# Kernel tuning notes

Measured on AMD Instinct MI355X. Metric: run time of the kernel, lower is better.

The kernel has to match this reference:

```python
import jax, jax.numpy as jnp
import numpy as np

B, N, M, D, H, DFF = 1, 2048, 2048, 1024, 16, 4096
MASK_VAL = -50000.0
EPS = 1e-5


def _xavier(k, shape):
    lim = np.sqrt(6.0 / (shape[0] + shape[1])).astype(np.float32)
    return jax.random.uniform(k, shape, jnp.float32, -lim, lim)


def setup_inputs() -> dict:
    key = jax.random.key(0)
    ks = jax.random.split(key, 8)
    return {
        "x": jax.random.normal(ks[0], (B, N, D), jnp.float32),
        "context": jax.random.normal(ks[1], (B, M, D), jnp.float32),
        "Wq": _xavier(ks[2], (D, D)), "bq": jnp.zeros((D,), jnp.float32),
        "Wkv": _xavier(ks[3], (D, 2 * D)), "bkv": jnp.zeros((2 * D,), jnp.float32),
        "Wo": _xavier(ks[4], (D, D)), "bo": jnp.zeros((D,), jnp.float32),
        "ln1_g": jnp.ones((D,), jnp.float32), "ln1_b": jnp.zeros((D,), jnp.float32),
        "W1": _xavier(ks[5], (D, DFF)), "bf1": jnp.zeros((DFF,), jnp.float32),
        "W2": _xavier(ks[6], (DFF, D)), "bf2": jnp.zeros((D,), jnp.float32),
        "ln2_g": jnp.ones((D,), jnp.float32), "ln2_b": jnp.zeros((D,), jnp.float32),
    }


def _layernorm(x, g, b):
    mu = x.mean(-1, keepdims=True)
    var = ((x - mu) ** 2).mean(-1, keepdims=True)
    return (x - mu) * jax.lax.rsqrt(var + EPS) * g + b


def reference(x, context, Wq, bq, Wkv, bkv, Wo, bo, ln1_g, ln1_b, W1, bf1, W2, bf2, ln2_g, ln2_b):
    b, n, d = x.shape
    m = context.shape[1]
    h = H
    dh = d // h
    scale = dh ** -0.5
    # q from x only; k,v from [x; context]
    q = (x @ Wq + bq).reshape(b, n, h, dh).transpose(0, 2, 1, 3)          # b h n dh
    kv_in = jnp.concatenate([x, context], axis=1)                          # b (n+m) d
    k, v = jnp.split(kv_in @ Wkv + bkv, 2, axis=-1)
    k = k.reshape(b, n + m, h, dh).transpose(0, 2, 1, 3)                   # b h (n+m) dh
    v = v.reshape(b, n + m, h, dh).transpose(0, 2, 1, 3)
    dots = jnp.einsum('bhid,bhjd->bhij', q * scale, k)                     # b h n (n+m)
    # causal mask applies only to the self-attention (first n) key columns
    rows = jnp.arange(n)[:, None]
    cols = jnp.arange(n + m)[None, :]
    causal = (cols < n) & (cols > rows)
    dots = jnp.where(causal, MASK_VAL, dots)
    attn = jax.nn.softmax(dots, axis=-1)                                   # dropout = identity (eval)
    out = jnp.einsum('bhij,bhjd->bhid', attn, v)
    out = out.transpose(0, 2, 1, 3).reshape(b, n, d) @ Wo + bo
    # PostNorm(Residual(attn))
    x1 = _layernorm(x + out, ln1_g, ln1_b)
    # PostNorm(Residual(FFN)) with exact-erf GELU
    ff = jax.nn.gelu(x1 @ W1 + bf1, approximate=False) @ W2 + bf2
    return _layernorm(x1 + ff, ln2_g, ln2_b)
```

## Files before the change

### kernel.cpp

```cpp
#include <hip/hip_runtime.h>


using bf16x8 = __attribute__((ext_vector_type(8))) short;
using f32x4  = __attribute__((ext_vector_type(4))) float;

__device__ __forceinline__ ushort f2bf(float f) {
    unsigned u = __float_as_uint(f);
    unsigned r = (u + 0x7fffu + ((u >> 16) & 1u)) >> 16;
    return (ushort)r;
}

__device__ __forceinline__ float bf2f(ushort u) {
    return __uint_as_float((uint)u << 16);
}

__device__ __forceinline__ void gload16(const void* g, void* l) {
    __builtin_amdgcn_global_load_lds(
        (const __attribute__((address_space(1))) void*)g,
        (__attribute__((address_space(3))) void*)l, 16, 0, 0);
}

__device__ __forceinline__ float gelu_erf(float v) {
    return 0.5f * v * (1.0f + erff(v * 0.70710678118654752f));
}

__device__ __forceinline__ uint cvtpk(float a, float b) {
    uint r;
    asm("v_cvt_pk_bf16_f32 %0, %1, %2" : "=v"(r) : "v"(a), "v"(b));
    return r;
}

__global__ __launch_bounds__(256) void prep_all(
    const float* __restrict__ x, const float* __restrict__ ctx,
    ushort* __restrict__ XCb,
    const float* __restrict__ Wq, const float* __restrict__ Wkv,
    const float* __restrict__ Wo, const float* __restrict__ W1,
    const float* __restrict__ W2,
    ushort* __restrict__ WqT, ushort* __restrict__ WkvT,
    ushort* __restrict__ WoT, ushort* __restrict__ W1T,
    ushort* __restrict__ W2T) {
    __shared__ float tile[32][33];
    int b = blockIdx.x;
    if (b < 4096) {
        const float* in = (b < 2048) ? x : ctx;
        ushort* out = XCb + ((b < 2048) ? 0 : (size_t)2048 * 1024);
        const int i = ((b & 2047) * 256 + threadIdx.x) * 4;
        float4 v = *(const float4*)(in + i);
        ushort4 o;
        o.x = f2bf(v.x); o.y = f2bf(v.y); o.z = f2bf(v.z); o.w = f2bf(v.w);
        *(ushort4*)(out + i) = o;
        return;
    }
    b -= 4096;
    const float* in; ushort* out; int R, C, loc;
    if (b < 1024)      { in = Wq;  out = WqT;  R = 1024; C = 1024; loc = b; }
    else if (b < 3072) { in = Wkv; out = WkvT; R = 1024; C = 2048; loc = b - 1024; }
    else if (b < 4096) { in = Wo;  out = WoT;  R = 1024; C = 1024; loc = b - 3072; }
    else if (b < 8192) { in = W1;  out = W1T;  R = 1024; C = 4096; loc = b - 4096; }
    else               { in = W2;  out = W2T;  R = 4096; C = 1024; loc = b - 8192; }
    const int nbx = C >> 5;
    const int c0 = (loc % nbx) * 32, r0 = (loc / nbx) * 32;
    const int tx = threadIdx.x & 31, ty = threadIdx.x >> 5;
#pragma unroll
    for (int i = 0; i < 4; ++i)
        tile[ty + 8 * i][tx] = in[(size_t)(r0 + ty + 8 * i) * C + c0 + tx];
    __syncthreads();
#pragma unroll
    for (int i = 0; i < 4; ++i)
        out[(size_t)(c0 + ty + 8 * i) * R + r0 + tx] = f2bf(tile[tx][ty + 8 * i]);
}

template <int BM, int BN, int ACT, int OUTF32, int RES, int SCALED, int SPLITK, int VT>
__global__ __launch_bounds__(256) void gemm_bt(
    const ushort* __restrict__ A, int lda, const ushort* __restrict__ Bt, int ldb,
    const float* __restrict__ bias, const float* __restrict__ resid,
    void* __restrict__ Cout, ushort* __restrict__ Vout,
    int M, int N, int K, float scale) {
    constexpr int MR = BM / 32, NR = BN / 32;
    __shared__ __align__(16) ushort Asm[BM * 64];
    __shared__ __align__(16) ushort Bsm[BN * 64];
    const int tid = threadIdx.x;
    const int w = tid >> 6, lane = tid & 63, g = lane >> 4, i15 = lane & 15;
    const int wm = w >> 1, wn = w & 1;
    const int m0 = blockIdx.y * BM, n0 = blockIdx.x * BN;
    if (SPLITK) {
        A += (size_t)blockIdx.z * K;
        Bt += (size_t)blockIdx.z * K;
    }

    f32x4 acc[MR][NR] = {};

    for (int kt = 0; kt < K; kt += 64) {
#pragma unroll
        for (int q = 0; q < BM / 32; ++q) {
            int off = (w * (BM / 32) + q) * 1024 + lane * 16;
            int r = off >> 7, cb = off & 127;
            int scb = cb ^ ((r & 7) << 4);
            const void* src = (const char*)A + ((size_t)(m0 + r) * lda + kt) * 2 + scb;
            gload16(src, (char*)Asm + (w * (BM / 32) + q) * 1024);
        }
#pragma unroll
        for (int q = 0; q < BN / 32; ++q) {
            int off = (w * (BN / 32) + q) * 1024 + lane * 16;
            int r = off >> 7, cb = off & 127;
            int scb = cb ^ ((r & 7) << 4);
            const void* src = (const char*)Bt + ((size_t)(n0 + r) * ldb + kt) * 2 + scb;
            gload16(src, (char*)Bsm + (w * (BN / 32) + q) * 1024);
        }
        __syncthreads();

#pragma unroll
        for (int kc = 0; kc < 2; ++kc) {
            bf16x8 af[MR], bfr[NR];
#pragma unroll
            for (int mi = 0; mi < MR; ++mi) {
                int r = wm * (BM / 2) + mi * 16 + i15;
                af[mi] = *(const bf16x8*)((const char*)Asm + r * 128 +
                                          ((kc * 64 + g * 16) ^ ((r & 7) << 4)));
            }
#pragma unroll
            for (int ni = 0; ni < NR; ++ni) {
                int r = wn * (BN / 2) + ni * 16 + i15;
                bfr[ni] = *(const bf16x8*)((const char*)Bsm + r * 128 +
                                           ((kc * 64 + g * 16) ^ ((r & 7) << 4)));
            }
#pragma unroll
            for (int mi = 0; mi < MR; ++mi)
#pragma unroll
                for (int ni = 0; ni < NR; ++ni)
                    acc[mi][ni] = __builtin_amdgcn_mfma_f32_16x16x32_bf16(
                        af[mi], bfr[ni], acc[mi][ni], 0, 0, 0);
        }
        __syncthreads();
    }

    float* Cf = (float*)Cout;
    ushort* Cb = (ushort*)Cout;
    if (SPLITK) {
        Cf += (size_t)blockIdx.z * M * N;
        Cb += (size_t)blockIdx.z * M * N;
    }

#pragma unroll
    for (int ni = 0; ni < NR; ++ni) {
        int col = n0 + wn * (BN / 2) + ni * 16 + i15;
        float bb = bias ? bias[col] : 0.f;
#pragma unroll
        for (int mi = 0; mi < MR; ++mi) {
            if (VT && col >= 1024) {
                int row = m0 + wm * (BM / 2) + mi * 16 + 4 * g;
                ushort4 ov;
                ov.x = f2bf(acc[mi][ni][0] + bb);
                ov.y = f2bf(acc[mi][ni][1] + bb);
                ov.z = f2bf(acc[mi][ni][2] + bb);
                ov.w = f2bf(acc[mi][ni][3] + bb);
                *(ushort4*)(Vout + (size_t)(col - 1024) * 4096 + row) = ov;
            } else {
#pragma unroll
                for (int r2 = 0; r2 < 4; ++r2) {
                    int row = m0 + wm * (BM / 2) + mi * 16 + 4 * g + r2;
                    float v = acc[mi][ni][r2] + bb;
                    if (ACT) v = gelu_erf(v);
                    if (SCALED) v *= scale;
                    size_t off = VT ? ((size_t)row * 1024 + col)
                                    : ((size_t)row * N + col);
                    if (OUTF32) {
                        float rv = RES ? resid[off] : 0.f;
                        Cf[off] = v + rv;
                    } else {
                        Cb[off] = f2bf(v);
                    }
                }
            }
        }
    }
}

template <int NS>
__global__ __launch_bounds__(512) void flash_attn(
    const ushort* __restrict__ Q,
    const ushort* __restrict__ Kb,
    const ushort* __restrict__ Vt,
    ushort* __restrict__ O,
    ushort* __restrict__ Opart,
    float* __restrict__ Ml) {
    constexpr int D = 1024;
    __shared__ __align__(16) ushort Ksm[2][64 * 64];
    __shared__ __align__(16) ushort Vsm[2][64 * 64];
    __shared__ __align__(16) ushort Psm[8][16 * 64];

    const int tid = threadIdx.x;
    const int w = tid >> 6, lane = tid & 63, g = lane >> 4, i15 = lane & 15;
    const int bid = blockIdx.x;
    const int h = bid & 15;
    const int qB = 15 - ((bid >> 4) & 15);
    const int s = (NS > 1) ? (bid >> 8) : 0;
    const int qb = qB * 128 + w * 16;
    const int qrow = qb + i15;
    const int diagW = qb >> 6;
    const int diagB = 2 * qB + 1;
    const int nt = diagB + 33;
    const int lo = (s * nt) / NS;
    const int hi = ((s + 1) * nt) / NS;

    bf16x8 qf[2];
    qf[0] = *(const bf16x8*)(Q + (size_t)qrow * D + h * 64 + g * 8);
    qf[1] = *(const bf16x8*)(Q + (size_t)qrow * D + h * 64 + 32 + g * 8);

    const short oneb = (short)0x3F80;
    const bf16x8 ones = {oneb, oneb, oneb, oneb, oneb, oneb, oneb, oneb};

    f32x4 o[4] = {};
    f32x4 ls = {};
    float m_run = -INFINITY;

    const int sr  = tid >> 3;
    const int scb = (tid & 7) * 16;
    const int ssw = scb ^ ((sr & 7) << 4);
    const char* kb0 = (const char*)Kb + ((size_t)sr * 1024 + h * 64) * 2 + scb;
    const char* vb0 = (const char*)Vt + ((size_t)(h * 64 + sr) * 4096) * 2 + scb;

    uint4 kreg, vreg;
    auto jt_of = [&](int t) { return (t <= diagB) ? t : (32 + (t - diagB - 1)); };
    auto stage = [&](int t) {
        const int jt = jt_of(t);
        kreg = *(const uint4*)(kb0 + (size_t)jt * 64 * 2048);
        vreg = *(const uint4*)(vb0 + (size_t)jt * 128);
    };
    auto wlds = [&](int buf) {
        *(uint4*)((char*)Ksm[buf] + sr * 128 + ssw) = kreg;
        *(uint4*)((char*)Vsm[buf] + sr * 128 + ssw) = vreg;
    };

    const int pbase = i15 * 128;
    const int psw = (i15 & 7) << 4;

    auto body = [&](int buf, int t) {
        const int jt = jt_of(t);
        f32x4 st[4];
        __builtin_amdgcn_s_setprio(1);
#pragma unroll
        for (int jg = 0; jg < 4; ++jg) {
            int jr = jg * 16 + i15;
            bf16x8 ka0 = *(const bf16x8*)((const char*)Ksm[buf] + jr * 128 +
                                          ((g * 16) ^ ((jr & 7) << 4)));
            bf16x8 ka1 = *(const bf16x8*)((const char*)Ksm[buf] + jr * 128 +
                                          ((64 + g * 16) ^ ((jr & 7) << 4)));
            f32x4 z = {};
            z = __builtin_amdgcn_mfma_f32_16x16x32_bf16(ka0, qf[0], z, 0, 0, 0);
            z = __builtin_amdgcn_mfma_f32_16x16x32_bf16(ka1, qf[1], z, 0, 0, 0);
            st[jg] = z;
        }
        __builtin_amdgcn_s_setprio(0);
        if (jt >= diagW && jt <= diagB) {
#pragma unroll
            for (int jg = 0; jg < 4; ++jg)
#pragma unroll
                for (int r = 0; r < 4; ++r) {
                    int j = jt * 64 + jg * 16 + 4 * g + r;
                    if (j > qrow) st[jg][r] = -50000.f;
                }
        }

        float a0 = fmaxf(fmaxf(st[0][0], st[0][1]), st[0][2]);
        float a1 = fmaxf(fmaxf(st[0][3], st[1][0]), st[1][1]);
        float a2 = fmaxf(fmaxf(st[1][2], st[1][3]), st[2][0]);
        float a3 = fmaxf(fmaxf(st[2][1], st[2][2]), st[2][3]);
        float a4 = fmaxf(fmaxf(st[3][0], st[3][1]), st[3][2]);
        float b0 = fmaxf(fmaxf(a0, a1), a2);
        float b1 = fmaxf(fmaxf(a3, a4), st[3][3]);
        float mt = fmaxf(b0, b1);
        mt = fmaxf(mt, __shfl_xor(mt, 16));
        mt = fmaxf(mt, __shfl_xor(mt, 32));

        const bool skip = __all(mt - m_run <= 8.f);
        float mnew, fscale;
        if (skip) { mnew = m_run; fscale = 1.f; }
        else      { mnew = fmaxf(m_run, mt); fscale = exp2f(m_run - mnew); }

        float pf[4][4];
#pragma unroll
        for (int jg = 0; jg < 4; ++jg)
#pragma unroll
            for (int r = 0; r < 4; ++r) pf[jg][r] = exp2f(st[jg][r] - mnew);
        m_run = mnew;

        if (!skip) {
#pragma unroll
            for (int r = 0; r < 4; ++r) {
                float fr = __shfl(fscale, 20 * g + r);
#pragma unroll
                for (int dg = 0; dg < 4; ++dg) o[dg][r] *= fr;
                ls[r] *= fr;
            }
        }

#pragma unroll
        for (int jg = 0; jg < 4; ++jg) {
            uint2 pk;
            pk.x = cvtpk(pf[jg][0], pf[jg][1]);
            pk.y = cvtpk(pf[jg][2], pf[jg][3]);
            *(uint2*)((char*)Psm[w] + pbase + ((jg * 32 + g * 8) ^ psw)) = pk;
        }

        __builtin_amdgcn_s_setprio(1);
#pragma unroll
        for (int jc = 0; jc < 2; ++jc) {
            bf16x8 pa = *(const bf16x8*)((const char*)Psm[w] + pbase +
                                         ((jc * 64 + g * 16) ^ psw));
            ls = __builtin_amdgcn_mfma_f32_16x16x32_bf16(pa, ones, ls, 0, 0, 0);
#pragma unroll
            for (int dg = 0; dg < 4; ++dg) {
                int dr = dg * 16 + i15;
                bf16x8 vb = *(const bf16x8*)((const char*)Vsm[buf] + dr * 128 +
                                             ((jc * 64 + g * 16) ^ ((dr & 7) << 4)));
                o[dg] = __builtin_amdgcn_mfma_f32_16x16x32_bf16(pa, vb, o[dg], 0, 0, 0);
            }
        }
        __builtin_amdgcn_s_setprio(0);
    };

    stage(lo);
    wlds(0);
    __syncthreads();

    int t = lo;
    for (; t + 1 < hi; t += 2) {
        stage(t + 1);
        body(0, t);
        wlds(1);
        __syncthreads();
        if (t + 2 < hi) stage(t + 2);
        body(1, t + 1);
        if (t + 2 < hi) { wlds(0); __syncthreads(); }
    }
    if (t < hi) body(0, t);

    if (NS > 1) {
#pragma unroll
        for (int r = 0; r < 4; ++r) {
            if (i15 == 4 * g + r) {
                float* mp = Ml + ((size_t)(s * 2048 + qrow) * 16 + h) * 2;
                mp[0] = m_run; mp[1] = ls[r];
            }
        }
#pragma unroll
        for (int r = 0; r < 4; ++r)
#pragma unroll
            for (int dg = 0; dg < 4; ++dg) {
                int row = qb + 4 * g + r;
                int col = h * 64 + dg * 16 + i15;
                Opart[(size_t)(s * 2048 + row) * 1024 + col] = f2bf(o[dg][r]);
            }
    } else {
#pragma unroll
        for (int r = 0; r < 4; ++r) {
            float inv = 1.f / ls[r];
#pragma unroll
            for (int dg = 0; dg < 4; ++dg) {
                int row = qb + 4 * g + r;
                int col = h * 64 + dg * 16 + i15;
                O[(size_t)row * D + col] = f2bf(o[dg][r] * inv);
            }
        }
    }
}

template <int NS>
__global__ __launch_bounds__(256) void attn_combine(
    const ushort* __restrict__ Opart, const float* __restrict__ Ml,
    ushort* __restrict__ O) {
    const int row = blockIdx.x, tid = threadIdx.x;
    const int c = tid * 4, h = c >> 6;
    float ms[NS], lsv[NS];
#pragma unroll
    for (int s = 0; s < NS; ++s) {
        const float* mp = Ml + ((size_t)(s * 2048 + row) * 16 + h) * 2;
        ms[s] = mp[0]; lsv[s] = mp[1];
    }
    float m = ms[0];
#pragma unroll
    for (int s = 1; s < NS; ++s) m = fmaxf(m, ms[s]);
    float denom = 0.f, wgt[NS];
#pragma unroll
    for (int s = 0; s < NS; ++s) { wgt[s] = exp2f(ms[s] - m); denom += lsv[s] * wgt[s]; }
    const float inv = 1.f / denom;
    float ax = 0, ay = 0, az = 0, aw = 0;
#pragma unroll
    for (int s = 0; s < NS; ++s) {
        ushort4 a = *(const ushort4*)(Opart + (size_t)(s * 2048 + row) * 1024 + c);
        ax += bf2f(a.x) * wgt[s]; ay += bf2f(a.y) * wgt[s];
        az += bf2f(a.z) * wgt[s]; aw += bf2f(a.w) * wgt[s];
    }
    ushort4 ob;
    ob.x = f2bf(ax * inv); ob.y = f2bf(ay * inv);
    ob.z = f2bf(az * inv); ob.w = f2bf(aw * inv);
    *(ushort4*)(O + (size_t)row * 1024 + c) = ob;
}

__global__ __launch_bounds__(256) void layernorm_k(
    const float* __restrict__ in, const float* __restrict__ gam,
    const float* __restrict__ bet, float* __restrict__ outf,
    ushort* __restrict__ outb) {
    const int row = blockIdx.x, tid = threadIdx.x;
    const float4 v = *(const float4*)(in + (size_t)row * 1024 + tid * 4);
    float s = v.x + v.y + v.z + v.w;
    float sq = v.x * v.x + v.y * v.y + v.z * v.z + v.w * v.w;
#pragma unroll
    for (int d = 1; d < 64; d <<= 1) {
        s += __shfl_xor(s, d);
        sq += __shfl_xor(sq, d);
    }
    __shared__ float red[8];
    const int w = tid >> 6;
    if ((tid & 63) == 0) { red[w] = s; red[4 + w] = sq; }
    __syncthreads();
    s = red[0] + red[1] + red[2] + red[3];
    sq = red[4] + red[5] + red[6] + red[7];
    const float mu = s * (1.f / 1024.f);
    const float rs = rsqrtf(sq * (1.f / 1024.f) - mu * mu + 1e-5f);
    const float4 gg = *(const float4*)(gam + tid * 4);
    const float4 bb = *(const float4*)(bet + tid * 4);
    float4 o;
    o.x = (v.x - mu) * rs * gg.x + bb.x;
    o.y = (v.y - mu) * rs * gg.y + bb.y;
    o.z = (v.z - mu) * rs * gg.z + bb.z;
    o.w = (v.w - mu) * rs * gg.w + bb.w;
    *(float4*)(outf + (size_t)row * 1024 + tid * 4) = o;
    if (outb) {
        ushort4 ob;
        ob.x = f2bf(o.x); ob.y = f2bf(o.y); ob.z = f2bf(o.z); ob.w = f2bf(o.w);
        *(ushort4*)(outb + (size_t)row * 1024 + tid * 4) = ob;
    }
}

template <int NP, int PBF16, int OUTB>
__global__ __launch_bounds__(256) void layernorm_comb(
    const void* __restrict__ P,
    const float* __restrict__ bias, const float* __restrict__ resid,
    const float* __restrict__ gam, const float* __restrict__ bet,
    float* __restrict__ outf, ushort* __restrict__ outb) {
    const int row = blockIdx.x, tid = threadIdx.x;
    const float4 rr = *(const float4*)(resid + (size_t)row * 1024 + tid * 4);
    const float4 bs = *(const float4*)(bias + tid * 4);
    float4 v;
    v.x = rr.x + bs.x; v.y = rr.y + bs.y; v.z = rr.z + bs.z; v.w = rr.w + bs.w;
#pragma unroll
    for (int p = 0; p < NP; ++p) {
        if (PBF16) {
            ushort4 a = *(const ushort4*)((const ushort*)P +
                          (size_t)(p * 2048 + row) * 1024 + tid * 4);
            v.x += bf2f(a.x); v.y += bf2f(a.y); v.z += bf2f(a.z); v.w += bf2f(a.w);
        } else {
            float4 a = *(const float4*)((const float*)P +
                          (size_t)(p * 2048 + row) * 1024 + tid * 4);
            v.x += a.x; v.y += a.y; v.z += a.z; v.w += a.w;
        }
    }
    float s = v.x + v.y + v.z + v.w;
    float sq = v.x * v.x + v.y * v.y + v.z * v.z + v.w * v.w;
#pragma unroll
    for (int d = 1; d < 64; d <<= 1) {
        s += __shfl_xor(s, d);
        sq += __shfl_xor(sq, d);
    }
    __shared__ float red[8];
    const int w = tid >> 6;
    if ((tid & 63) == 0) { red[w] = s; red[4 + w] = sq; }
    __syncthreads();
    s = red[0] + red[1] + red[2] + red[3];
    sq = red[4] + red[5] + red[6] + red[7];
    const float mu = s * (1.f / 1024.f);
    const float rs = rsqrtf(sq * (1.f / 1024.f) - mu * mu + 1e-5f);
    const float4 gg = *(const float4*)(gam + tid * 4);
    const float4 bb = *(const float4*)(bet + tid * 4);
    float4 o;
    o.x = (v.x - mu) * rs * gg.x + bb.x;
    o.y = (v.y - mu) * rs * gg.y + bb.y;
    o.z = (v.z - mu) * rs * gg.z + bb.z;
    o.w = (v.w - mu) * rs * gg.w + bb.w;
    *(float4*)(outf + (size_t)row * 1024 + tid * 4) = o;
    if (OUTB) {
        ushort4 ob;
        ob.x = f2bf(o.x); ob.y = f2bf(o.y); ob.z = f2bf(o.z); ob.w = f2bf(o.w);
        *(ushort4*)(outb + (size_t)row * 1024 + tid * 4) = ob;
    }
}

extern "C" void kernel_launch(void* const* d_in, const int* in_sizes, int n_in,
                              void* d_out, int out_size, void* d_ws, size_t ws_size,
                              hipStream_t stream) {
    const float* x    = (const float*)d_in[0];
    const float* ctx  = (const float*)d_in[1];
    const float* Wq   = (const float*)d_in[2];
    const float* bq   = (const float*)d_in[3];
    const float* Wkv  = (const float*)d_in[4];
    const float* bkv  = (const float*)d_in[5];
    const float* Wo   = (const float*)d_in[6];
    const float* bo   = (const float*)d_in[7];
    const float* g1   = (const float*)d_in[8];
    const float* b1   = (const float*)d_in[9];
    const float* W1   = (const float*)d_in[10];
    const float* bf1  = (const float*)d_in[11];
    const float* W2   = (const float*)d_in[12];
    const float* bf2  = (const float*)d_in[13];
    const float* g2   = (const float*)d_in[14];
    const float* b2   = (const float*)d_in[15];

    char* ws = (char*)d_ws;
    const size_t MB = 1u << 20;
    ushort* XCb  = (ushort*)(ws + 0);
    ushort* WoT  = (ushort*)(ws + 8 * MB);
    ushort* W1T  = (ushort*)(ws + 10 * MB);
    ushort* W2T  = (ushort*)(ws + 18 * MB);
    ushort* WqT  = (ushort*)(ws + 26 * MB);
    ushort* WkvT = (ushort*)(ws + 28 * MB);
    ushort* Qs   = (ushort*)(ws + 32 * MB);
    ushort* attn = (ushort*)(ws + 36 * MB);
    ushort* Kb   = (ushort*)(ws + 40 * MB);
    ushort* Vt   = (ushort*)(ws + 48 * MB);
    ushort* x1b  = (ushort*)(ws + 26 * MB);
    float*  x1f  = (float*)(ws + 32 * MB);
    ushort* ffb  = (ushort*)(ws + 40 * MB);
    float*  y1   = (float*)(ws + 56 * MB);
    ushort* Opart = (ushort*)(ws + 64 * MB);
    float*  Pwo   = (float*)(ws + 64 * MB);
    ushort* Pk4b  = (ushort*)(ws + 64 * MB);
    float*  Pk2   = (float*)(ws + 0);
    float*  Ml    = (float*)(ws + 80 * MB);

    prep_all<<<16384, 256, 0, stream>>>(x, ctx, XCb, Wq, Wkv, Wo, W1, W2,
                                        WqT, WkvT, WoT, W1T, W2T);
    gemm_bt<64, 128, 0, 0, 0, 1, 0, 0><<<dim3(8, 32), 256, 0, stream>>>(
        XCb, 1024, WqT, 1024, bq, nullptr, Qs, nullptr,
        2048, 1024, 1024, 0.18033688011112042f);
    gemm_bt<128, 128, 0, 0, 0, 0, 0, 1><<<dim3(16, 32), 256, 0, stream>>>(
        XCb, 1024, WkvT, 1024, bkv, nullptr, Kb, Vt,
        4096, 2048, 1024, 1.f);

    const bool big = ws_size >= 82 * MB;
    if (big) {
        flash_attn<4><<<1024, 512, 0, stream>>>(Qs, Kb, Vt, nullptr, Opart, Ml);
        attn_combine<4><<<2048, 256, 0, stream>>>(Opart, Ml, attn);
        gemm_bt<64, 128, 0, 1, 0, 0, 1, 0><<<dim3(8, 32, 2), 256, 0, stream>>>(
            attn, 1024, WoT, 1024, nullptr, nullptr, Pwo, nullptr,
            2048, 1024, 512, 1.f);
        layernorm_comb<2, 0, 1><<<2048, 256, 0, stream>>>(
            Pwo, bo, x, g1, b1, x1f, x1b);
        gemm_bt<128, 128, 1, 0, 0, 0, 0, 0><<<dim3(32, 16), 256, 0, stream>>>(
            x1b, 1024, W1T, 1024, bf1, nullptr, ffb, nullptr,
            2048, 4096, 1024, 1.f);
        gemm_bt<128, 128, 0, 0, 0, 0, 1, 0><<<dim3(8, 16, 4), 256, 0, stream>>>(
            ffb, 4096, W2T, 4096, nullptr, nullptr, Pk4b, nullptr,
            2048, 1024, 1024, 1.f);
        layernorm_comb<4, 1, 0><<<2048, 256, 0, stream>>>(
            Pk4b, bf2, x1f, g2, b2, (float*)d_out, nullptr);
    } else {
        flash_attn<1><<<256, 512, 0, stream>>>(Qs, Kb, Vt, attn, nullptr, nullptr);
        gemm_bt<64, 128, 0, 1, 1, 0, 0, 0><<<dim3(8, 32), 256, 0, stream>>>(
            attn, 1024, WoT, 1024, bo, x, y1, nullptr, 2048, 1024, 1024, 1.f);
        layernorm_k<<<2048, 256, 0, stream>>>(y1, g1, b1, x1f, x1b);
        gemm_bt<128, 128, 1, 0, 0, 0, 0, 0><<<dim3(32, 16), 256, 0, stream>>>(
            x1b, 1024, W1T, 1024, bf1, nullptr, ffb, nullptr,
            2048, 4096, 1024, 1.f);
        gemm_bt<128, 128, 0, 1, 0, 0, 1, 0><<<dim3(8, 16, 2), 256, 0, stream>>>(
            ffb, 4096, W2T, 4096, nullptr, nullptr, Pk2, nullptr,
            2048, 1024, 2048, 1.f);
        layernorm_comb<2, 0, 0><<<2048, 256, 0, stream>>>(
            Pk2, bf2, x1f, g2, b2, (float*)d_out, nullptr);
    }
}
```

Measured before the change: 204.4 us.

## Fuse Q and KV projections into one GEMM launch; vectorize weight transpose

Replaces the separate Q projection GEMM and KV projection GEMM with a single gemm_qkv kernel. It uses a flat 640-block grid: 128 blocks cover the Q region over the first 2048 rows and 512 blocks cover the K/V region over all 4096 rows. Each block picks its output (scaled Q, K, or transposed V) from its column range. This removes one launch and lets both projections fill the GPU together. The weight-transpose prep now uses float4 loads and packed bf16 stores via v_cvt_pk_bf16_f32, cutting memory instructions. It assumes WqT and WkvT are contiguous in the workspace so one Bt pointer covers the concatenated 3072-column weight.

Result: no change. 207.0 us (+1.3%).

```diff
diff --git a/kernel.cpp b/kernel.cpp
--- a/kernel.cpp
+++ b/kernel.cpp
@@ -41,10 +41,11 @@
     ushort* __restrict__ W2T) {
     __shared__ float tile[32][33];
     int b = blockIdx.x;
+    const int t = threadIdx.x;
     if (b < 4096) {
         const float* in = (b < 2048) ? x : ctx;
         ushort* out = XCb + ((b < 2048) ? 0 : (size_t)2048 * 1024);
-        const int i = ((b & 2047) * 256 + threadIdx.x) * 4;
+        const int i = ((b & 2047) * 256 + t) * 4;
         float4 v = *(const float4*)(in + i);
         ushort4 o;
         o.x = f2bf(v.x); o.y = f2bf(v.y); o.z = f2bf(v.z); o.w = f2bf(v.w);
@@ -60,22 +61,27 @@
     else               { in = W2;  out = W2T;  R = 4096; C = 1024; loc = b - 8192; }
     const int nbx = C >> 5;
     const int c0 = (loc % nbx) * 32, r0 = (loc / nbx) * 32;
-    const int tx = threadIdx.x & 31, ty = threadIdx.x >> 5;
-#pragma unroll
-    for (int i = 0; i < 4; ++i)
-        tile[ty + 8 * i][tx] = in[(size_t)(r0 + ty + 8 * i) * C + c0 + tx];
+    {
+        const int r = t >> 3, c4 = (t & 7) * 4;
+        float4 v = *(const float4*)(in + (size_t)(r0 + r) * C + c0 + c4);
+        tile[r][c4] = v.x; tile[r][c4 + 1] = v.y;
+        tile[r][c4 + 2] = v.z; tile[r][c4 + 3] = v.w;
+    }
     __syncthreads();
-#pragma unroll
-    for (int i = 0; i < 4; ++i)
-        out[(size_t)(c0 + ty + 8 * i) * R + r0 + tx] = f2bf(tile[tx][ty + 8 * i]);
-}
-
-template <int BM, int BN, int ACT, int OUTF32, int RES, int SCALED, int SPLITK, int VT>
+    {
+        const int c = t >> 3, r4 = (t & 7) * 4;
+        uint2 pk;
+        pk.x = cvtpk(tile[r4][c], tile[r4 + 1][c]);
+        pk.y = cvtpk(tile[r4 + 2][c], tile[r4 + 3][c]);
+        *(uint2*)(out + (size_t)(c0 + c) * R + r0 + r4) = pk;
+    }
+}
+
+template <int BM, int BN, int ACT, int OUTF32, int RES, int SCALED, int SPLITK>
 __global__ __launch_bounds__(256) void gemm_bt(
     const ushort* __restrict__ A, int lda, const ushort* __restrict__ Bt, int ldb,
     const float* __restrict__ bias, const float* __restrict__ resid,
-    void* __restrict__ Cout, ushort* __restrict__ Vout,
-    int M, int N, int K, float scale) {
+    void* __restrict__ Cout, int M, int N, int K, float scale) {
     constexpr int MR = BM / 32, NR = BN / 32;
     __shared__ __align__(16) ushort Asm[BM * 64];
     __shared__ __align__(16) ushort Bsm[BN * 64];
@@ -147,28 +153,112 @@
         float bb = bias ? bias[col] : 0.f;
 #pragma unroll
         for (int mi = 0; mi < MR; ++mi) {
-            if (VT && col >= 1024) {
-                int row = m0 + wm * (BM / 2) + mi * 16 + 4 * g;
+#pragma unroll
+            for (int r2 = 0; r2 < 4; ++r2) {
+                int row = m0 + wm * (BM / 2) + mi * 16 + 4 * g + r2;
+                float v = acc[mi][ni][r2] + bb;
+                if (ACT) v = gelu_erf(v);
+                if (SCALED) v *= scale;
+                size_t off = (size_t)row * N + col;
+                if (OUTF32) {
+                    float rv = RES ? resid[off] : 0.f;
+                    Cf[off] = v + rv;
+                } else {
+                    Cb[off] = f2bf(v);
+                }
+            }
+        }
+    }
+}
+
+__global__ __launch_bounds__(256) void gemm_qkv(
+    const ushort* __restrict__ A,
+    const ushort* __restrict__ Bt,
+    const float* __restrict__ bq, const float* __restrict__ bkv,
+    ushort* __restrict__ Qs, ushort* __restrict__ Kb, ushort* __restrict__ Vt,
+    float qscale) {
+    constexpr int MR = 4, NR = 4;
+    __shared__ __align__(16) ushort Asm[128 * 64];
+    __shared__ __align__(16) ushort Bsm[128 * 64];
+    const int tid = threadIdx.x;
+    const int w = tid >> 6, lane = tid & 63, g = lane >> 4, i15 = lane & 15;
+    const int wm = w >> 1, wn = w & 1;
+    const int bid = blockIdx.x;
+    int bx, by;
+    if (bid < 128) { bx = bid & 7; by = bid >> 3; }
+    else { int b2 = bid - 128; bx = 8 + (b2 & 15); by = b2 >> 4; }
+    const int m0 = by * 128, n0 = bx * 128;
+    const int reg = (n0 < 1024) ? 0 : (n0 < 2048 ? 1 : 2);
+
+    f32x4 acc[MR][NR] = {};
+
+    for (int kt = 0; kt < 1024; kt += 64) {
+#pragma unroll
+        for (int q = 0; q < 4; ++q) {
+            int off = (w * 4 + q) * 1024 + lane * 16;
+            int r = off >> 7, cb = off & 127;
+            int scb = cb ^ ((r & 7) << 4);
+            const void* src = (const char*)A + ((size_t)(m0 + r) * 1024 + kt) * 2 + scb;
+            gload16(src, (char*)Asm + (w * 4 + q) * 1024);
+        }
+#pragma unroll
+        for (int q = 0; q < 4; ++q) {
+            int off = (w * 4 + q) * 1024 + lane * 16;
+            int r = off >> 7, cb = off & 127;
+            int scb = cb ^ ((r & 7) << 4);
+            const void* src = (const char*)Bt + ((size_t)(n0 + r) * 1024 + kt) * 2 + scb;
+            gload16(src, (char*)Bsm + (w * 4 + q) * 1024);
+        }
+        __syncthreads();
+
+#pragma unroll
+        for (int kc = 0; kc < 2; ++kc) {
+            bf16x8 af[MR], bfr[NR];
+#pragma unroll
+            for (int mi = 0; mi < MR; ++mi) {
+                int r = wm * 64 + mi * 16 + i15;
+                af[mi] = *(const bf16x8*)((const char*)Asm + r * 128 +
+                                          ((kc * 64 + g * 16) ^ ((r & 7) << 4)));
+            }
+#pragma unroll
+            for (int ni = 0; ni < NR; ++ni) {
+                int r = wn * 64 + ni * 16 + i15;
+                bfr[ni] = *(const bf16x8*)((const char*)Bsm + r * 128 +
+                                           ((kc * 64 + g * 16) ^ ((r & 7) << 4)));
+            }
+#pragma unroll
+            for (int mi = 0; mi < MR; ++mi)
+#pragma unroll
+                for (int ni = 0; ni < NR; ++ni)
+                    acc[mi][ni] = __builtin_amdgcn_mfma_f32_16x16x32_bf16(
+                        af[mi], bfr[ni], acc[mi][ni], 0, 0, 0);
+        }
+        __syncthreads();
+    }
+
+#pragma unroll
+    for (int ni = 0; ni < NR; ++ni) {
+        int col = n0 + wn * 64 + ni * 16 + i15;
+        float bb = (reg == 0) ? bq[col] : bkv[col - 1024];
+#pragma unroll
+        for (int mi = 0; mi < MR; ++mi) {
+            if (reg == 2) {
+                int row = m0 + wm * 64 + mi * 16 + 4 * g;
                 ushort4 ov;
                 ov.x = f2bf(acc[mi][ni][0] + bb);
                 ov.y = f2bf(acc[mi][ni][1] + bb);
                 ov.z = f2bf(acc[mi][ni][2] + bb);
                 ov.w = f2bf(acc[mi][ni][3] + bb);
-                *(ushort4*)(Vout + (size_t)(col - 1024) * 4096 + row) = ov;
+                *(ushort4*)(Vt + (size_t)(col - 2048) * 4096 + row) = ov;
             } else {
 #pragma unroll
                 for (int r2 = 0; r2 < 4; ++r2) {
-                    int row = m0 + wm * (BM / 2) + mi * 16 + 4 * g + r2;
+                    int row = m0 + wm * 64 + mi * 16 + 4 * g + r2;
                     float v = acc[mi][ni][r2] + bb;
-                    if (ACT) v = gelu_erf(v);
-                    if (SCALED) v *= scale;
-                    size_t off = VT ? ((size_t)row * 1024 + col)
-                                    : ((size_t)row * N + col);
-                    if (OUTF32) {
-                        float rv = RES ? resid[off] : 0.f;
-                        Cf[off] = v + rv;
+                    if (reg == 0) {
+                        Qs[(size_t)row * 1024 + col] = f2bf(v * qscale);
                     } else {
-                        Cb[off] = f2bf(v);
+                        Kb[(size_t)row * 1024 + (col - 1024)] = f2bf(v);
                     }
                 }
             }
@@ -531,41 +621,35 @@
 
     prep_all<<<16384, 256, 0, stream>>>(x, ctx, XCb, Wq, Wkv, Wo, W1, W2,
                                         WqT, WkvT, WoT, W1T, W2T);
-    gemm_bt<64, 128, 0, 0, 0, 1, 0, 0><<<dim3(8, 32), 256, 0, stream>>>(
-        XCb, 1024, WqT, 1024, bq, nullptr, Qs, nullptr,
-        2048, 1024, 1024, 0.18033688011112042f);
-    gemm_bt<128, 128, 0, 0, 0, 0, 0, 1><<<dim3(16, 32), 256, 0, stream>>>(
-        XCb, 1024, WkvT, 1024, bkv, nullptr, Kb, Vt,
-        4096, 2048, 1024, 1.f);
+    gemm_qkv<<<640, 256, 0, stream>>>(XCb, WqT, bq, bkv, Qs, Kb, Vt,
+                                      0.18033688011112042f);
 
     const bool big = ws_size >= 82 * MB;
     if (big) {
         flash_attn<4><<<1024, 512, 0, stream>>>(Qs, Kb, Vt, nullptr, Opart, Ml);
         attn_combine<4><<<2048, 256, 0, stream>>>(Opart, Ml, attn);
-        gemm_bt<64, 128, 0, 1, 0, 0, 1, 0><<<dim3(8, 32, 2), 256, 0, stream>>>(
-            attn, 1024, WoT, 1024, nullptr, nullptr, Pwo, nullptr,
+        gemm_bt<64, 128, 0, 1, 0, 0, 1><<<dim3(8, 32, 2), 256, 0, stream>>>(
+            attn, 1024, WoT, 1024, nullptr, nullptr, Pwo,
             2048, 1024, 512, 1.f);
         layernorm_comb<2, 0, 1><<<2048, 256, 0, stream>>>(
             Pwo, bo, x, g1, b1, x1f, x1b);
-        gemm_bt<128, 128, 1, 0, 0, 0, 0, 0><<<dim3(32, 16), 256, 0, stream>>>(
-            x1b, 1024, W1T, 1024, bf1, nullptr, ffb, nullptr,
+        gemm_bt<128, 128, 1, 0, 0, 0, 0><<<dim3(32, 16), 256, 0, stream>>>(
+            x1b, 1024, W1T, 1024, bf1, nullptr, ffb,
             2048, 4096, 1024, 1.f);
-        gemm_bt<128, 128, 0, 0, 0, 0, 1, 0><<<dim3(8, 16, 4), 256, 0, stream>>>(
-            ffb, 4096, W2T, 4096, nullptr, nullptr, Pk4b, nullptr,
+        gemm_bt<128, 128, 0, 0, 0, 0, 1><<<dim3(8, 16, 4), 256, 0, stream>>>(
+            ffb, 4096, W2T, 4096, nullptr, nullptr, Pk4b,
             2048, 1024, 1024, 1.f);
         layernorm_comb<4, 1, 0><<<2048, 256, 0, stream>>>(
             Pk4b, bf2, x1f, g2, b2, (float*)d_out, nullptr);
     } else {
         flash_attn<1><<<256, 512, 0, stream>>>(Qs, Kb, Vt, attn, nullptr, nullptr);
-        gemm_bt<64, 128, 0, 1, 1, 0, 0, 0><<<dim3(8, 32), 256, 0, stream>>>(
-            attn, 1024, WoT, 1024, bo, x, y1, nullptr, 2048, 1024, 1024, 1.f);
+        gemm_bt<64, 128, 0, 1, 1, 0, 0><<<dim3(8, 32), 256, 0, stream>>>(
+            attn, 1024, WoT, 1024, bo, x, y1, 2048, 1024, 1024, 1.f);
         layernorm_k<<<2048, 256, 0, stream>>>(y1, g1, b1, x1f, x1b);
-        gemm_bt<128, 128, 1, 0, 0, 0, 0, 0><<<dim3(32, 16), 256, 0, stream>>>(
-            x1b, 1024, W1T, 1024, bf1, nullptr, ffb, nullptr,
-            2048, 4096, 1024, 1.f);
-        gemm_bt<128, 128, 0, 1, 0, 0, 1, 0><<<dim3(8, 16, 2), 256, 0, stream>>>(
-            ffb, 4096, W2T, 4096, nullptr, nullptr, Pk2, nullptr,
-            2048, 1024, 2048, 1.f);
+        gemm_bt<128, 128, 1, 0, 0, 0, 0><<<dim3(32, 16), 256, 0, stream>>>(
+            x1b, 1024, W1T, 1024, bf1, nullptr, ffb, 2048, 4096, 1024, 1.f);
+        gemm_bt<128, 128, 0, 1, 0, 0, 1><<<dim3(8, 16, 2), 256, 0, stream>>>(
+            ffb, 4096, W2T, 4096, nullptr, nullptr, Pk2, 2048, 1024, 2048, 1.f);
         layernorm_comb<2, 0, 0><<<2048, 256, 0, stream>>>(
             Pk2, bf2, x1f, g2, b2, (float*)d_out, nullptr);
     }
```
